# Optimization experiments

Hardware: AMD Instinct MI355X
Metric: run time of the kernel (lower is better)

## Reference

```python
import jax, jax.numpy as jnp
import numpy as np

POI_LEN = 38333
FEAT = 898
EMBED = 128
OUT_DIM = 128
K = 1  # masked entries per node (mask has exactly K True per row)
E = POI_LEN * 32


def _glorot(key, shape):
    fan_in = shape[0]
    return jax.random.normal(key, shape, jnp.float32) / np.float32(np.sqrt(fan_in))


def setup_inputs() -> dict:
    key = jax.random.key(0)
    ks = jax.random.split(key, 16)
    x = jax.random.normal(ks[0], (POI_LEN, FEAT), jnp.float32)
    # column 0 holds POI ids (as floats), selected by the mask
    ids = jax.random.randint(ks[1], (POI_LEN,), 0, POI_LEN, jnp.int32)
    x = x.at[:, 0].set(ids.astype(jnp.float32))
    mask = jnp.zeros((POI_LEN, FEAT), jnp.bool_).at[:, 0].set(True)
    edge_index = jax.random.randint(ks[2], (2, E), 0, POI_LEN, jnp.int32)
    return {
        "x": x,
        "edge_index": edge_index,
        "mask": mask,
        "emb": jax.random.normal(ks[3], (POI_LEN, EMBED), jnp.float32),
        "W1": _glorot(ks[4], (FEAT, 64)), "b1": jnp.zeros((64,), jnp.float32),
        "W2": _glorot(ks[5], (64, 32)), "b2": jnp.zeros((32,), jnp.float32),
        "W3": _glorot(ks[6], (32, 32)), "b3": jnp.zeros((32,), jnp.float32),
        "W4": _glorot(ks[7], (32, 32)), "b4": jnp.zeros((32,), jnp.float32),
        "W5": _glorot(ks[8], (32, 1)), "b5": jnp.zeros((1,), jnp.float32),
        "fcW1": _glorot(ks[9], (POI_LEN, 128)), "fcb1": jnp.zeros((128,), jnp.float32),
        "fcW2": _glorot(ks[10], (128, OUT_DIM)), "fcb2": jnp.zeros((OUT_DIM,), jnp.float32),
    }


def reference(x, edge_index, mask, emb, W1, b1, W2, b2, W3, b3, W4, b4, W5, b5,
              fcW1, fcb1, fcW2, fcb2):
    N, F = x.shape
    # --- masked_select -> poi ids; embedding; masked_scatter back ---
    mask_flat = mask.reshape(-1)
    # stable argsort puts True positions first, in row-major order
    order = jnp.argsort(jnp.logical_not(mask_flat), stable=True)
    M = N * K  # number of True entries (static)
    sel = order[:M]
    poi = x.reshape(-1)[sel].astype(jnp.int32)       # [M] poi ids
    emb_poi = emb[poi.reshape(N, K)]                  # [N, K, EMBED]
    # masked_scatter: fill the M True slots with the first M source elements
    feat = x.reshape(-1).at[sel].set(emb_poi.reshape(-1)[:M]).reshape(N, F)
    # --- GCN normalization with self-loops (PyG GCNConv default) ---
    loops = jnp.arange(N, dtype=edge_index.dtype)
    src = jnp.concatenate([edge_index[0], loops])
    dst = jnp.concatenate([edge_index[1], loops])
    deg = jax.ops.segment_sum(jnp.ones(src.shape, feat.dtype), dst, num_segments=N)
    dis = jnp.where(deg > 0, jax.lax.rsqrt(jnp.maximum(deg, 1.0)), 0.0)
    norm = (dis[src] * dis[dst])[:, None]             # [E+N, 1]

    def gcn(h, W, b):
        h = h @ W                                     # [N, out]
        agg = jax.ops.segment_sum(h[src] * norm, dst, num_segments=N)
        return agg + b

    lrelu = lambda v: jax.nn.leaky_relu(v, 0.01)
    h = lrelu(gcn(feat, W1, b1))
    h = lrelu(gcn(h, W2, b2))
    t = gcn(h, W3, b3)
    h = lrelu(t) + t
    t = gcn(h, W4, b4)
    h = lrelu(t) + t
    h = lrelu(gcn(h, W5, b5)).reshape(-1)             # [N]
    out = jax.nn.relu(h @ fcW1 + fcb1)
    out = jax.nn.relu(out @ fcW2 + fcb2)              # [OUT_DIM]
    return out
```

## Files before the change

### kernel.cpp

```cpp
#include <hip/hip_runtime.h>
#include <math.h>

#define NPOI 38333
#define FEATD 898
#define EMBD 128

__global__ __launch_bounds__(256) void init_kernel(const float* __restrict__ x,
                                                   const float* __restrict__ emb,
                                                   float* __restrict__ c0,
                                                   int* __restrict__ cnt) {
  int i = blockIdx.x * 256 + threadIdx.x;
  if (i < NPOI) {
    int id = (int)x[(size_t)(i >> 7) * FEATD];
    c0[i] = emb[(size_t)id * EMBD + (i & 127)];
    cnt[i] = 0;
  }
}

__global__ __launch_bounds__(256) void hist_kernel(const int* __restrict__ dst,
                                                   int* __restrict__ cnt, int E) {
  int e = blockIdx.x * 256 + threadIdx.x;
  if (e < E) atomicAdd(&cnt[dst[e]], 1);
}

__global__ __launch_bounds__(256) void dis_kernel(const int* __restrict__ cnt,
                                                  float* __restrict__ dis) {
  int i = blockIdx.x * 256 + threadIdx.x;
  if (i < NPOI) dis[i] = 1.0f / sqrtf((float)(cnt[i] + 1));
}

__global__ __launch_bounds__(1024) void scan_kernel(const int* __restrict__ cnt,
                                                    int* __restrict__ rs,
                                                    int* __restrict__ cur) {
  const int t = threadIdx.x;
  const int CH = (NPOI + 1023) >> 10;
  int lo = t * CH, hi = lo + CH;
  if (lo > NPOI) lo = NPOI;
  if (hi > NPOI) hi = NPOI;
  int s = 0;
  for (int i = lo; i < hi; ++i) s += cnt[i];
  const int lane = t & 63, wid = t >> 6;
  int v = s;
#pragma unroll
  for (int d = 1; d < 64; d <<= 1) {
    int u = __shfl_up(v, d, 64);
    if (lane >= d) v += u;
  }
  __shared__ int wsum[16];
  __shared__ int woff[17];
  if (lane == 63) wsum[wid] = v;
  __syncthreads();
  if (t == 0) {
    int run = 0;
    for (int i = 0; i < 16; ++i) { woff[i] = run; run += wsum[i]; }
    woff[16] = run;
  }
  __syncthreads();
  int run = woff[wid] + v - s;
  for (int i = lo; i < hi; ++i) {
    rs[i] = run;
    cur[i] = 0;
    run += cnt[i];
  }
  if (t == 1023) rs[NPOI] = woff[16];
}

__global__ __launch_bounds__(256) void fill_kernel(const int* __restrict__ src,
                                                   const int* __restrict__ dst,
                                                   const float* __restrict__ dis,
                                                   const int* __restrict__ rs,
                                                   int* __restrict__ cur,
                                                   int* __restrict__ neigh,
                                                   float* __restrict__ nw, int E) {
  int e = blockIdx.x * 256 + threadIdx.x;
  if (e >= E) return;
  int d = dst[e], s = src[e];
  int pos = rs[d] + atomicAdd(&cur[d], 1);
  neigh[pos] = s;
  nw[pos] = dis[s];
}

__global__ __launch_bounds__(256) void gemm1_kernel(const float* __restrict__ x,
                                                    const float* __restrict__ c0,
                                                    const float* __restrict__ W1,
                                                    float* __restrict__ p0,
                                                    float* __restrict__ p1) {
  const int b = blockIdx.x;
  const int rb = b >> 1, ks = b & 1;
  const int row0 = rb * 32;
  const int kbeg = ks ? 448 : 0;
  const int kend = ks ? FEATD : 448;
  float* outp = ks ? p1 : p0;

  __shared__ float As[32][36];
  __shared__ float Bs[32][68];

  const int tid = threadIdx.x;
  const int tx = tid & 15, ty = tid >> 4;
  float acc[2][4] = {{0, 0, 0, 0}, {0, 0, 0, 0}};

  for (int kb = kbeg; kb < kend; kb += 32) {
#pragma unroll
    for (int l = tid; l < 512; l += 256) {
      int m = l >> 4, kh = l & 15;
      int row = row0 + m, kg = kb + kh * 2;
      float2 v = {0.0f, 0.0f};
      if (row < NPOI && kg < kend) {
        v = *(const float2*)&x[(size_t)row * FEATD + kg];
        if (kg == 0) v.x = c0[row];
      }
      *(float2*)&As[m][kh * 2] = v;
    }
#pragma unroll
    for (int l = tid; l < 512; l += 256) {
      int kk = l >> 4, n4 = l & 15;
      int kg = kb + kk;
      float4 v = {0.0f, 0.0f, 0.0f, 0.0f};
      if (kg < kend) v = *(const float4*)&W1[(size_t)kg * 64 + n4 * 4];
      *(float4*)&Bs[kk][n4 * 4] = v;
    }
    __syncthreads();
#pragma unroll
    for (int k4 = 0; k4 < 8; ++k4) {
      const float4 a0 = *(const float4*)&As[ty * 2 + 0][k4 * 4];
      const float4 a1 = *(const float4*)&As[ty * 2 + 1][k4 * 4];
      const float4 b0 = *(const float4*)&Bs[k4 * 4 + 0][tx * 4];
      const float4 b1 = *(const float4*)&Bs[k4 * 4 + 1][tx * 4];
      const float4 b2 = *(const float4*)&Bs[k4 * 4 + 2][tx * 4];
      const float4 b3 = *(const float4*)&Bs[k4 * 4 + 3][tx * 4];
      acc[0][0] += a0.x * b0.x + a0.y * b1.x + a0.z * b2.x + a0.w * b3.x;
      acc[0][1] += a0.x * b0.y + a0.y * b1.y + a0.z * b2.y + a0.w * b3.y;
      acc[0][2] += a0.x * b0.z + a0.y * b1.z + a0.z * b2.z + a0.w * b3.z;
      acc[0][3] += a0.x * b0.w + a0.y * b1.w + a0.z * b2.w + a0.w * b3.w;
      acc[1][0] += a1.x * b0.x + a1.y * b1.x + a1.z * b2.x + a1.w * b3.x;
      acc[1][1] += a1.x * b0.y + a1.y * b1.y + a1.z * b2.y + a1.w * b3.y;
      acc[1][2] += a1.x * b0.z + a1.y * b1.z + a1.z * b2.z + a1.w * b3.z;
      acc[1][3] += a1.x * b0.w + a1.y * b1.w + a1.z * b2.w + a1.w * b3.w;
    }
    __syncthreads();
  }
#pragma unroll
  for (int i = 0; i < 2; ++i) {
    int row = row0 + ty * 2 + i;
    if (row < NPOI) {
      float4 v = {acc[i][0], acc[i][1], acc[i][2], acc[i][3]};
      *(float4*)&outp[(size_t)row * 64 + tx * 4] = v;
    }
  }
}

__global__ __launch_bounds__(256) void combine_kernel(float* __restrict__ p0,
                                                      const float* __restrict__ p1,
                                                      int n4) {
  int i = blockIdx.x * 256 + threadIdx.x;
  if (i >= n4) return;
  float4 a = ((const float4*)p0)[i];
  float4 b = ((const float4*)p1)[i];
  a.x += b.x; a.y += b.y; a.z += b.z; a.w += b.w;
  ((float4*)p0)[i] = a;
}

template <int ACT>
__global__ __launch_bounds__(256) void gather64_kernel(const float* __restrict__ hw,
                                                       const float* __restrict__ dis,
                                                       const int* __restrict__ rs,
                                                       const int* __restrict__ neigh,
                                                       const float* __restrict__ nw,
                                                       const float* __restrict__ b,
                                                       float* __restrict__ out) {
  int node = blockIdx.x * 4 + (threadIdx.x >> 6);
  if (node >= NPOI) return;
  int f = threadIdx.x & 63;
  float dd = dis[node];
  float acc = dd * hw[(size_t)node * 64 + f];
  int j = rs[node];
  const int j1 = rs[node + 1];
  for (; j + 3 < j1; j += 4) {
    int s0 = neigh[j], s1 = neigh[j + 1], s2 = neigh[j + 2], s3 = neigh[j + 3];
    float w0 = nw[j], w1 = nw[j + 1], w2 = nw[j + 2], w3 = nw[j + 3];
    acc += w0 * hw[(size_t)s0 * 64 + f];
    acc += w1 * hw[(size_t)s1 * 64 + f];
    acc += w2 * hw[(size_t)s2 * 64 + f];
    acc += w3 * hw[(size_t)s3 * 64 + f];
  }
  for (; j < j1; ++j) acc += nw[j] * hw[(size_t)neigh[j] * 64 + f];
  float v = dd * acc + b[f];
  float l = v > 0.0f ? v : 0.01f * v;
  out[(size_t)node * 64 + f] = ACT ? (l + v) : l;
}

template <int ACT>
__global__ __launch_bounds__(256) void gather32_kernel(const float* __restrict__ hw,
                                                       const float* __restrict__ dis,
                                                       const int* __restrict__ rs,
                                                       const int* __restrict__ neigh,
                                                       const float* __restrict__ nw,
                                                       const float* __restrict__ b,
                                                       float* __restrict__ out) {
  int node = blockIdx.x * 8 + (threadIdx.x >> 5);
  if (node >= NPOI) return;
  int f = threadIdx.x & 31;
  float dd = dis[node];
  float acc = dd * hw[(size_t)node * 32 + f];
  int j = rs[node];
  const int j1 = rs[node + 1];
  for (; j + 3 < j1; j += 4) {
    int s0 = neigh[j], s1 = neigh[j + 1], s2 = neigh[j + 2], s3 = neigh[j + 3];
    float w0 = nw[j], w1 = nw[j + 1], w2 = nw[j + 2], w3 = nw[j + 3];
    acc += w0 * hw[(size_t)s0 * 32 + f];
    acc += w1 * hw[(size_t)s1 * 32 + f];
    acc += w2 * hw[(size_t)s2 * 32 + f];
    acc += w3 * hw[(size_t)s3 * 32 + f];
  }
  for (; j < j1; ++j) acc += nw[j] * hw[(size_t)neigh[j] * 32 + f];
  float v = dd * acc + b[f];
  float l = v > 0.0f ? v : 0.01f * v;
  out[(size_t)node * 32 + f] = ACT ? (l + v) : l;
}

__global__ __launch_bounds__(256) void gather1_kernel(const float* __restrict__ h5w,
                                                      const float* __restrict__ dis,
                                                      const int* __restrict__ rs,
                                                      const int* __restrict__ neigh,
                                                      const float* __restrict__ nw,
                                                      const float* __restrict__ b5,
                                                      float* __restrict__ out) {
  int node = blockIdx.x * 4 + (threadIdx.x >> 6);
  if (node >= NPOI) return;
  int lane = threadIdx.x & 63;
  float dd = dis[node];
  float acc = 0.0f;
  const int j0 = rs[node], j1 = rs[node + 1];
  for (int j = j0 + lane; j < j1; j += 64) acc += nw[j] * h5w[neigh[j]];
#pragma unroll
  for (int d = 32; d > 0; d >>= 1) acc += __shfl_down(acc, d, 64);
  if (lane == 0) {
    float v = dd * (acc + dd * h5w[node]) + b5[0];
    out[node] = v > 0.0f ? v : 0.01f * v;
  }
}

template <int KIN>
__global__ __launch_bounds__(256) void gemm_small32(const float* __restrict__ h,
                                                    const float* __restrict__ W,
                                                    float* __restrict__ out) {
  __shared__ float Ws[KIN * 32];
  __shared__ float Hs[8][KIN];
  const int tid = threadIdx.x;
  const int row0 = blockIdx.x * 8;
  for (int l = tid; l < KIN * 32; l += 256) Ws[l] = W[l];
  for (int l = tid; l < 8 * KIN; l += 256) {
    int r = l / KIN, k = l % KIN;
    int row = row0 + r;
    Hs[r][k] = (row < NPOI) ? h[(size_t)row * KIN + k] : 0.0f;
  }
  __syncthreads();
  const int r = tid >> 5, c = tid & 31;
  float acc = 0.0f;
#pragma unroll
  for (int k = 0; k < KIN; ++k) acc += Hs[r][k] * Ws[k * 32 + c];
  int row = row0 + r;
  if (row < NPOI) out[(size_t)row * 32 + c] = acc;
}

__global__ __launch_bounds__(256) void gemm_w5(const float* __restrict__ h,
                                               const float* __restrict__ W5,
                                               float* __restrict__ out) {
  __shared__ float Ws[32];
  if (threadIdx.x < 32) Ws[threadIdx.x] = W5[threadIdx.x];
  __syncthreads();
  int i = blockIdx.x * 256 + threadIdx.x;
  if (i >= NPOI) return;
  float acc = 0.0f;
#pragma unroll
  for (int k = 0; k < 32; ++k) acc += h[(size_t)i * 32 + k] * Ws[k];
  out[i] = acc;
}

__global__ __launch_bounds__(128) void matvec_kernel(const float* __restrict__ h5,
                                                     const float* __restrict__ fcW1,
                                                     float* __restrict__ part) {
  int j = threadIdx.x;
  int b = blockIdx.x;
  int i0 = b * 64, iend = i0 + 64;
  if (iend > NPOI) iend = NPOI;
  float a0 = 0.0f, a1 = 0.0f, a2 = 0.0f, a3 = 0.0f;
  int i = i0;
  for (; i + 3 < iend; i += 4) {
    a0 += h5[i + 0] * fcW1[(size_t)(i + 0) * 128 + j];
    a1 += h5[i + 1] * fcW1[(size_t)(i + 1) * 128 + j];
    a2 += h5[i + 2] * fcW1[(size_t)(i + 2) * 128 + j];
    a3 += h5[i + 3] * fcW1[(size_t)(i + 3) * 128 + j];
  }
  for (; i < iend; ++i) a0 += h5[i] * fcW1[(size_t)i * 128 + j];
  part[(size_t)b * 128 + j] = (a0 + a1) + (a2 + a3);
}

__global__ __launch_bounds__(64) void reduce_kernel(const float* __restrict__ part,
                                                    int npart,
                                                    const float* __restrict__ fcb1,
                                                    float* __restrict__ h1) {
  const int j = blockIdx.x;
  const int lane = threadIdx.x;
  float acc = 0.0f;
  for (int b = lane; b < npart; b += 64) acc += part[(size_t)b * 128 + j];
#pragma unroll
  for (int d = 32; d > 0; d >>= 1) acc += __shfl_down(acc, d, 64);
  if (lane == 0) {
    float v = acc + fcb1[j];
    h1[j] = v > 0.0f ? v : 0.0f;
  }
}

__global__ __launch_bounds__(64) void head2_kernel(const float* __restrict__ h1,
                                                   const float* __restrict__ fcW2,
                                                   const float* __restrict__ fcb2,
                                                   float* __restrict__ out) {
  const int t = blockIdx.x;
  const int lane = threadIdx.x;
  float acc = h1[lane] * fcW2[(size_t)lane * 128 + t] +
              h1[lane + 64] * fcW2[(size_t)(lane + 64) * 128 + t];
#pragma unroll
  for (int d = 32; d > 0; d >>= 1) acc += __shfl_down(acc, d, 64);
  if (lane == 0) {
    float v = acc + fcb2[t];
    out[t] = v > 0.0f ? v : 0.0f;
  }
}

extern "C" void kernel_launch(void* const* d_in, const int* in_sizes, int n_in,
                              void* d_out, int out_size, void* d_ws, size_t ws_size,
                              hipStream_t stream) {
  const float* x    = (const float*)d_in[0];
  const int*   ei   = (const int*)d_in[1];
  const float* emb  = (const float*)d_in[3];
  const float* W1   = (const float*)d_in[4];
  const float* b1   = (const float*)d_in[5];
  const float* W2   = (const float*)d_in[6];
  const float* b2   = (const float*)d_in[7];
  const float* W3   = (const float*)d_in[8];
  const float* b3   = (const float*)d_in[9];
  const float* W4   = (const float*)d_in[10];
  const float* b4   = (const float*)d_in[11];
  const float* W5   = (const float*)d_in[12];
  const float* b5   = (const float*)d_in[13];
  const float* fcW1 = (const float*)d_in[14];
  const float* fcb1 = (const float*)d_in[15];
  const float* fcW2 = (const float*)d_in[16];
  const float* fcb2 = (const float*)d_in[17];
  float* out = (float*)d_out;

  const int E = in_sizes[1] / 2;
  const int* srcE = ei;
  const int* dstE = ei + E;

  float* ws = (float*)d_ws;
  size_t off = 0;
  auto carve = [&](size_t n) {
    float* p = ws + off;
    off += (n + 255) & ~(size_t)255;
    return p;
  };
  float* c0    = carve(NPOI);
  float* dis   = carve(NPOI);
  int*   cnt   = (int*)carve(NPOI);
  int*   rs    = (int*)carve(NPOI + 1);
  int*   cur   = (int*)carve(NPOI);
  int*   neigh = (int*)carve(E);
  float* nw    = carve(E);
  float* p0    = carve((size_t)NPOI * 64);
  float* p1    = carve((size_t)NPOI * 64);
  float* bufH  = carve((size_t)NPOI * 64);
  const int NMV = (NPOI + 63) / 64;
  float* part  = carve((size_t)NMV * 128);
  float* h1    = carve(128);
  (void)ws_size; (void)n_in; (void)out_size;

  const int gN    = (NPOI + 255) / 256;
  const int gE    = (E + 255) / 256;
  const int gG64  = (NPOI + 3) / 4;
  const int gG32  = (NPOI + 7) / 8;
  const int gS    = (NPOI + 7) / 8;
  const int RB1   = (NPOI + 31) / 32;
  const int n4    = (NPOI * 64) / 4;
  const int gC    = (n4 + 255) / 256;

  init_kernel<<<gN, 256, 0, stream>>>(x, emb, c0, cnt);
  hist_kernel<<<gE, 256, 0, stream>>>(dstE, cnt, E);
  scan_kernel<<<1, 1024, 0, stream>>>(cnt, rs, cur);
  dis_kernel<<<gN, 256, 0, stream>>>(cnt, dis);
  fill_kernel<<<gE, 256, 0, stream>>>(srcE, dstE, dis, rs, cur, neigh, nw, E);

  gemm1_kernel<<<RB1 * 2, 256, 0, stream>>>(x, c0, W1, p0, p1);
  combine_kernel<<<gC, 256, 0, stream>>>(p0, p1, n4);
  gather64_kernel<0><<<gG64, 256, 0, stream>>>(p0, dis, rs, neigh, nw, b1, bufH);

  gemm_small32<64><<<gS, 256, 0, stream>>>(bufH, W2, p0);
  gather32_kernel<0><<<gG32, 256, 0, stream>>>(p0, dis, rs, neigh, nw, b2, bufH);

  gemm_small32<32><<<gS, 256, 0, stream>>>(bufH, W3, p0);
  gather32_kernel<1><<<gG32, 256, 0, stream>>>(p0, dis, rs, neigh, nw, b3, bufH);

  gemm_small32<32><<<gS, 256, 0, stream>>>(bufH, W4, p0);
  gather32_kernel<1><<<gG32, 256, 0, stream>>>(p0, dis, rs, neigh, nw, b4, bufH);

  gemm_w5<<<gN, 256, 0, stream>>>(bufH, W5, p0);
  gather1_kernel<<<gG64, 256, 0, stream>>>(p0, dis, rs, neigh, nw, b5, c0);

  matvec_kernel<<<NMV, 128, 0, stream>>>(c0, fcW1, part);
  reduce_kernel<<<128, 64, 0, stream>>>(part, NMV, fcb1, h1);
  head2_kernel<<<128, 64, 0, stream>>>(h1, fcW2, fcb2, out);
}
```

Measured before the change: 774.8 us.

## Replace FP32 layer-1 GEMM with split-bf16 MFMA kernel and in-block K reduction

The first GCN GEMM (38333x898 by 898x64) now runs on MFMA bf16 instructions. Both operands are split into hi and lo bf16 parts and three products are accumulated to approximate fp32 accuracy. W1 is pre-split and transposed once by a small kernel. The two K halves are computed by separate half-blocks and reduced through shared memory, which removes the partial buffer and the combine kernel. The gather loops are also unrolled to 8 neighbours to expose more memory-level parallelism, at some cost in precision (about fp32 minus a few bits) and extra conversion work per element.

Result: faster. 733.8 us (-5.3%).

```diff
diff --git a/kernel.cpp b/kernel.cpp
--- a/kernel.cpp
+++ b/kernel.cpp
@@ -4,6 +4,12 @@
 #define NPOI 38333
 #define FEATD 898
 #define EMBD 128
+#define KPAD 928
+#define NKT 29
+#define SPLIT0 15
+
+typedef short s16x8 __attribute__((ext_vector_type(8)));
+typedef float f32x4 __attribute__((ext_vector_type(4)));
 
 __global__ __launch_bounds__(256) void init_kernel(const float* __restrict__ x,
                                                    const float* __restrict__ emb,
@@ -27,6 +33,21 @@
                                                   float* __restrict__ dis) {
   int i = blockIdx.x * 256 + threadIdx.x;
   if (i < NPOI) dis[i] = 1.0f / sqrtf((float)(cnt[i] + 1));
+}
+
+__global__ __launch_bounds__(256) void wsplit_kernel(const float* __restrict__ W1,
+                                                     unsigned short* __restrict__ WhiT,
+                                                     unsigned short* __restrict__ WloT) {
+  int n = blockIdx.x;
+  for (int k = threadIdx.x; k < KPAD; k += 256) {
+    float f = (k < FEATD) ? W1[(size_t)k * 64 + n] : 0.0f;
+    unsigned b = __float_as_uint(f);
+    unsigned hb = b & 0xFFFF0000u;
+    float r = f - __uint_as_float(hb);
+    unsigned rb = __float_as_uint(r) & 0xFFFF0000u;
+    WhiT[(size_t)n * KPAD + k] = (unsigned short)(hb >> 16);
+    WloT[(size_t)n * KPAD + k] = (unsigned short)(rb >> 16);
+  }
 }
 
 __global__ __launch_bounds__(1024) void scan_kernel(const int* __restrict__ cnt,
@@ -80,84 +101,98 @@
   nw[pos] = dis[s];
 }
 
-__global__ __launch_bounds__(256) void gemm1_kernel(const float* __restrict__ x,
-                                                    const float* __restrict__ c0,
-                                                    const float* __restrict__ W1,
-                                                    float* __restrict__ p0,
-                                                    float* __restrict__ p1) {
-  const int b = blockIdx.x;
-  const int rb = b >> 1, ks = b & 1;
-  const int row0 = rb * 32;
-  const int kbeg = ks ? 448 : 0;
-  const int kend = ks ? FEATD : 448;
-  float* outp = ks ? p1 : p0;
-
-  __shared__ float As[32][36];
-  __shared__ float Bs[32][68];
+__global__ __launch_bounds__(512) void gemm1_mfma(const float* __restrict__ x,
+                                                  const float* __restrict__ c0,
+                                                  const unsigned short* __restrict__ WhiT,
+                                                  const unsigned short* __restrict__ WloT,
+                                                  float* __restrict__ out) {
+  __shared__ unsigned short smem[2][4][64][40];
 
   const int tid = threadIdx.x;
-  const int tx = tid & 15, ty = tid >> 4;
-  float acc[2][4] = {{0, 0, 0, 0}, {0, 0, 0, 0}};
-
-  for (int kb = kbeg; kb < kend; kb += 32) {
-#pragma unroll
-    for (int l = tid; l < 512; l += 256) {
-      int m = l >> 4, kh = l & 15;
-      int row = row0 + m, kg = kb + kh * 2;
-      float2 v = {0.0f, 0.0f};
-      if (row < NPOI && kg < kend) {
-        v = *(const float2*)&x[(size_t)row * FEATD + kg];
-        if (kg == 0) v.x = c0[row];
+  const int half = tid >> 8;
+  const int t = tid & 255;
+  const int row0 = blockIdx.x * 64;
+  const int wv = (tid >> 6) & 3;
+  const int lane = tid & 63;
+  const int m16 = lane & 15, kg = lane >> 4;
+
+  f32x4 acc[4] = {};
+
+  const int kt0 = half ? SPLIT0 : 0;
+  const int kt1 = half ? NKT : SPLIT0;
+
+  for (int it = 0; it < SPLIT0; ++it) {
+    const int kt = kt0 + it;
+    const bool active = kt < kt1;
+    if (active) {
+      const int k0 = kt * 32;
+#pragma unroll
+      for (int i = 0; i < 4; ++i) {
+        int fid = t + i * 256;
+        int row = fid >> 4, kq2 = fid & 15;
+        int k = k0 + kq2 * 2;
+        float2 v = {0.0f, 0.0f};
+        int grow = row0 + row;
+        if (grow < NPOI && k < FEATD) {
+          v = *(const float2*)&x[(size_t)grow * FEATD + k];
+          if (k == 0) v.x = c0[grow];
+        }
+        unsigned b0 = __float_as_uint(v.x), b1 = __float_as_uint(v.y);
+        unsigned h0 = b0 & 0xFFFF0000u, h1 = b1 & 0xFFFF0000u;
+        float r0 = v.x - __uint_as_float(h0);
+        float r1 = v.y - __uint_as_float(h1);
+        unsigned l0 = __float_as_uint(r0) & 0xFFFF0000u;
+        unsigned l1 = __float_as_uint(r1) & 0xFFFF0000u;
+        *(unsigned*)&smem[half][0][row][kq2 * 2] = (h0 >> 16) | h1;
+        *(unsigned*)&smem[half][1][row][kq2 * 2] = (l0 >> 16) | l1;
       }
-      *(float2*)&As[m][kh * 2] = v;
-    }
-#pragma unroll
-    for (int l = tid; l < 512; l += 256) {
-      int kk = l >> 4, n4 = l & 15;
-      int kg = kb + kk;
-      float4 v = {0.0f, 0.0f, 0.0f, 0.0f};
-      if (kg < kend) v = *(const float4*)&W1[(size_t)kg * 64 + n4 * 4];
-      *(float4*)&Bs[kk][n4 * 4] = v;
+#pragma unroll
+      for (int i = 0; i < 2; ++i) {
+        int fid = t + i * 256;
+        int col = fid >> 3, kq = fid & 7;
+        int k = kt * 32 + kq * 4;
+        *(uint2*)&smem[half][2][col][kq * 4] =
+            *(const uint2*)&WhiT[(size_t)col * KPAD + k];
+        *(uint2*)&smem[half][3][col][kq * 4] =
+            *(const uint2*)&WloT[(size_t)col * KPAD + k];
+      }
     }
     __syncthreads();
-#pragma unroll
-    for (int k4 = 0; k4 < 8; ++k4) {
-      const float4 a0 = *(const float4*)&As[ty * 2 + 0][k4 * 4];
-      const float4 a1 = *(const float4*)&As[ty * 2 + 1][k4 * 4];
-      const float4 b0 = *(const float4*)&Bs[k4 * 4 + 0][tx * 4];
-      const float4 b1 = *(const float4*)&Bs[k4 * 4 + 1][tx * 4];
-      const float4 b2 = *(const float4*)&Bs[k4 * 4 + 2][tx * 4];
-      const float4 b3 = *(const float4*)&Bs[k4 * 4 + 3][tx * 4];
-      acc[0][0] += a0.x * b0.x + a0.y * b1.x + a0.z * b2.x + a0.w * b3.x;
-      acc[0][1] += a0.x * b0.y + a0.y * b1.y + a0.z * b2.y + a0.w * b3.y;
-      acc[0][2] += a0.x * b0.z + a0.y * b1.z + a0.z * b2.z + a0.w * b3.z;
-      acc[0][3] += a0.x * b0.w + a0.y * b1.w + a0.z * b2.w + a0.w * b3.w;
-      acc[1][0] += a1.x * b0.x + a1.y * b1.x + a1.z * b2.x + a1.w * b3.x;
-      acc[1][1] += a1.x * b0.y + a1.y * b1.y + a1.z * b2.y + a1.w * b3.y;
-      acc[1][2] += a1.x * b0.z + a1.y * b1.z + a1.z * b2.z + a1.w * b3.z;
-      acc[1][3] += a1.x * b0.w + a1.y * b1.w + a1.z * b2.w + a1.w * b3.w;
+    if (active) {
+      s16x8 a_hi = *(const s16x8*)&smem[half][0][wv * 16 + m16][kg * 8];
+      s16x8 a_lo = *(const s16x8*)&smem[half][1][wv * 16 + m16][kg * 8];
+#pragma unroll
+      for (int g = 0; g < 4; ++g) {
+        s16x8 b_hi = *(const s16x8*)&smem[half][2][g * 16 + m16][kg * 8];
+        s16x8 b_lo = *(const s16x8*)&smem[half][3][g * 16 + m16][kg * 8];
+        acc[g] = __builtin_amdgcn_mfma_f32_16x16x32_bf16(a_hi, b_hi, acc[g], 0, 0, 0);
+        acc[g] = __builtin_amdgcn_mfma_f32_16x16x32_bf16(a_hi, b_lo, acc[g], 0, 0, 0);
+        acc[g] = __builtin_amdgcn_mfma_f32_16x16x32_bf16(a_lo, b_hi, acc[g], 0, 0, 0);
+      }
     }
     __syncthreads();
   }
-#pragma unroll
-  for (int i = 0; i < 2; ++i) {
-    int row = row0 + ty * 2 + i;
-    if (row < NPOI) {
-      float4 v = {acc[i][0], acc[i][1], acc[i][2], acc[i][3]};
-      *(float4*)&outp[(size_t)row * 64 + tx * 4] = v;
-    }
-  }
-}
-
-__global__ __launch_bounds__(256) void combine_kernel(float* __restrict__ p0,
-                                                      const float* __restrict__ p1,
-                                                      int n4) {
-  int i = blockIdx.x * 256 + threadIdx.x;
-  if (i >= n4) return;
-  float4 a = ((const float4*)p0)[i];
-  float4 b = ((const float4*)p1)[i];
-  a.x += b.x; a.y += b.y; a.z += b.z; a.w += b.w;
-  ((float4*)p0)[i] = a;
+
+  float (*red)[64] = (float(*)[64])smem;
+  if (half == 1) {
+#pragma unroll
+    for (int g = 0; g < 4; ++g)
+#pragma unroll
+      for (int r = 0; r < 4; ++r)
+        red[wv * 16 + kg * 4 + r][g * 16 + m16] = acc[g][r];
+  }
+  __syncthreads();
+  if (half == 0) {
+#pragma unroll
+    for (int g = 0; g < 4; ++g)
+#pragma unroll
+      for (int r = 0; r < 4; ++r) {
+        int grow = row0 + wv * 16 + kg * 4 + r;
+        if (grow < NPOI)
+          out[(size_t)grow * 64 + g * 16 + m16] =
+              acc[g][r] + red[wv * 16 + kg * 4 + r][g * 16 + m16];
+      }
+  }
 }
 
 template <int ACT>
@@ -175,13 +210,19 @@
   float acc = dd * hw[(size_t)node * 64 + f];
   int j = rs[node];
   const int j1 = rs[node + 1];
-  for (; j + 3 < j1; j += 4) {
+  for (; j + 7 < j1; j += 8) {
     int s0 = neigh[j], s1 = neigh[j + 1], s2 = neigh[j + 2], s3 = neigh[j + 3];
+    int s4 = neigh[j + 4], s5 = neigh[j + 5], s6 = neigh[j + 6], s7 = neigh[j + 7];
     float w0 = nw[j], w1 = nw[j + 1], w2 = nw[j + 2], w3 = nw[j + 3];
+    float w4 = nw[j + 4], w5 = nw[j + 5], w6 = nw[j + 6], w7 = nw[j + 7];
     acc += w0 * hw[(size_t)s0 * 64 + f];
     acc += w1 * hw[(size_t)s1 * 64 + f];
     acc += w2 * hw[(size_t)s2 * 64 + f];
     acc += w3 * hw[(size_t)s3 * 64 + f];
+    acc += w4 * hw[(size_t)s4 * 64 + f];
+    acc += w5 * hw[(size_t)s5 * 64 + f];
+    acc += w6 * hw[(size_t)s6 * 64 + f];
+    acc += w7 * hw[(size_t)s7 * 64 + f];
   }
   for (; j < j1; ++j) acc += nw[j] * hw[(size_t)neigh[j] * 64 + f];
   float v = dd * acc + b[f];
@@ -204,13 +245,19 @@
   float acc = dd * hw[(size_t)node * 32 + f];
   int j = rs[node];
   const int j1 = rs[node + 1];
-  for (; j + 3 < j1; j += 4) {
+  for (; j + 7 < j1; j += 8) {
     int s0 = neigh[j], s1 = neigh[j + 1], s2 = neigh[j + 2], s3 = neigh[j + 3];
+    int s4 = neigh[j + 4], s5 = neigh[j + 5], s6 = neigh[j + 6], s7 = neigh[j + 7];
     float w0 = nw[j], w1 = nw[j + 1], w2 = nw[j + 2], w3 = nw[j + 3];
+    float w4 = nw[j + 4], w5 = nw[j + 5], w6 = nw[j + 6], w7 = nw[j + 7];
     acc += w0 * hw[(size_t)s0 * 32 + f];
     acc += w1 * hw[(size_t)s1 * 32 + f];
     acc += w2 * hw[(size_t)s2 * 32 + f];
     acc += w3 * hw[(size_t)s3 * 32 + f];
+    acc += w4 * hw[(size_t)s4 * 32 + f];
+    acc += w5 * hw[(size_t)s5 * 32 + f];
+    acc += w6 * hw[(size_t)s6 * 32 + f];
+    acc += w7 * hw[(size_t)s7 * 32 + f];
   }
   for (; j < j1; ++j) acc += nw[j] * hw[(size_t)neigh[j] * 32 + f];
   float v = dd * acc + b[f];
@@ -368,8 +415,9 @@
   int*   cur   = (int*)carve(NPOI);
   int*   neigh = (int*)carve(E);
   float* nw    = carve(E);
+  unsigned short* WhiT = (unsigned short*)carve(64 * KPAD / 2);
+  unsigned short* WloT = (unsigned short*)carve(64 * KPAD / 2);
   float* p0    = carve((size_t)NPOI * 64);
-  float* p1    = carve((size_t)NPOI * 64);
   float* bufH  = carve((size_t)NPOI * 64);
   const int NMV = (NPOI + 63) / 64;
   float* part  = carve((size_t)NMV * 128);
@@ -381,18 +429,16 @@
   const int gG64  = (NPOI + 3) / 4;
   const int gG32  = (NPOI + 7) / 8;
   const int gS    = (NPOI + 7) / 8;
-  const int RB1   = (NPOI + 31) / 32;
-  const int n4    = (NPOI * 64) / 4;
-  const int gC    = (n4 + 255) / 256;
+  const int GB1   = (NPOI + 63) / 64;
 
   init_kernel<<<gN, 256, 0, stream>>>(x, emb, c0, cnt);
   hist_kernel<<<gE, 256, 0, stream>>>(dstE, cnt, E);
   scan_kernel<<<1, 1024, 0, stream>>>(cnt, rs, cur);
   dis_kernel<<<gN, 256, 0, stream>>>(cnt, dis);
   fill_kernel<<<gE, 256, 0, stream>>>(srcE, dstE, dis, rs, cur, neigh, nw, E);
-
-  gemm1_kernel<<<RB1 * 2, 256, 0, stream>>>(x, c0, W1, p0, p1);
-  combine_kernel<<<gC, 256, 0, stream>>>(p0, p1, n4);
+  wsplit_kernel<<<64, 256, 0, stream>>>(W1, WhiT, WloT);
+
+  gemm1_mfma<<<GB1, 512, 0, stream>>>(x, c0, WhiT, WloT, p0);
   gather64_kernel<0><<<gG64, 256, 0, stream>>>(p0, dis, rs, neigh, nw, b1, bufH);
 
   gemm_small32<64><<<gS, 256, 0, stream>>>(bufH, W2, p0);
```
